# Optimization experiments

Hardware: AMD Instinct MI355X
Metric: run time of the kernel (lower is better)

The kernel has to match this reference:

```python
import jax, jax.numpy as jnp
import numpy as np

N_NODES = 100000


def gcn_layer(x, src, dst, W, b):
    """PyG GCNConv: add self-loops, symmetric deg normalization, XW then scatter-add."""
    n = x.shape[0]
    loop = jnp.arange(n, dtype=src.dtype)
    s = jnp.concatenate([src, loop])
    d = jnp.concatenate([dst, loop])
    # degree of target nodes (includes self-loop)
    deg = jax.ops.segment_sum(jnp.ones_like(d, dtype=x.dtype), d, num_segments=n)
    dinv = jnp.where(deg > 0, jax.lax.rsqrt(deg), 0.0)
    norm = dinv[s] * dinv[d]                      # [E+N]
    h = x @ W                                     # [N, out]
    msg = h[s] * norm[:, None]                    # [E+N, out]
    out = jax.ops.segment_sum(msg, d, num_segments=n) + b
    return out


def setup_inputs() -> dict:
    key = jax.random.key(0)
    k1, k2, k3, k4 = jax.random.split(key, 4)
    d_in, d_hid, d_out = 256, 256, 128
    E = 3200000
    x = jax.random.normal(k1, (N_NODES, d_in), dtype=jnp.float32)
    edge_index = jax.random.randint(k2, (2, E), 0, N_NODES, dtype=jnp.int64)
    # glorot-style init for GCN weights
    W1 = jax.random.normal(k3, (d_in, d_hid), dtype=jnp.float32) / np.sqrt(d_in)
    b1 = jnp.zeros((d_hid,), dtype=jnp.float32)
    W2 = jax.random.normal(k4, (d_hid, d_out), dtype=jnp.float32) / np.sqrt(d_hid)
    b2 = jnp.zeros((d_out,), dtype=jnp.float32)
    return {"x": x, "W1": W1, "b1": b1, "W2": W2, "b2": b2, "edge_index": edge_index}


def reference(x, W1, b1, W2, b2, edge_index):
    src, dst = edge_index[0], edge_index[1]
    h = jax.nn.relu(gcn_layer(x, src, dst, W1, b1))
    out = jax.nn.relu(gcn_layer(h, src, dst, W2, b2))
    return out
```

## Files before the change

kernel.cpp:

```cpp
#include <hip/hip_runtime.h>


typedef short          s16x8 __attribute__((ext_vector_type(8)));
typedef float          f32x4 __attribute__((ext_vector_type(4)));
typedef unsigned short u16x8 __attribute__((ext_vector_type(8)));
typedef unsigned short u16x4 __attribute__((ext_vector_type(4)));

__device__ __forceinline__ float bf2f(unsigned short u) {
  union { unsigned int i; float f; } x; x.i = ((unsigned int)u) << 16; return x.f;
}
__device__ __forceinline__ unsigned short f2bf(float f) {
  union { float f; unsigned int i; } x; x.f = f;
  unsigned int r = x.i + 0x7FFFu + ((x.i >> 16) & 1u);
  return (unsigned short)(r >> 16);
}


#define NBUCK_PAD 1024
#define BIN_CHUNK 8192

__global__ __launch_bounds__(256) void k_hist(const int* __restrict__ dst,
                                              int* __restrict__ bcnt, int E) {
  __shared__ int h[NBUCK_PAD];
  int t = threadIdx.x;
  for (int i = t; i < NBUCK_PAD; i += 256) h[i] = 0;
  __syncthreads();
  int stride = gridDim.x * 256;
  for (int e = blockIdx.x * 256 + t; e < E; e += stride) atomicAdd(&h[dst[e] >> 7], 1);
  __syncthreads();
  for (int i = t; i < NBUCK_PAD; i += 256) {
    int v = h[i];
    if (v) atomicAdd(bcnt + i, v);
  }
}

__global__ void k_bscan(const int* __restrict__ bcnt, int* __restrict__ bptr,
                        int* __restrict__ bcur, int* __restrict__ rowptr, int M, int E) {
  __shared__ int sh[NBUCK_PAD];
  int t = threadIdx.x;
  int v = bcnt[t];
  sh[t] = v; __syncthreads();
  int x = v;
  for (int off = 1; off < NBUCK_PAD; off <<= 1) {
    int y = (t >= off) ? sh[t - off] : 0;
    __syncthreads();
    x += y; sh[t] = x;
    __syncthreads();
  }
  bptr[t] = x - v;
  bcur[t] = x - v;
  if (t == NBUCK_PAD - 1) bptr[NBUCK_PAD] = x;
  if (t == 0) rowptr[M] = E;
}

__global__ __launch_bounds__(256) void k_bin(const int* __restrict__ src,
                                             const int* __restrict__ dst,
                                             int* __restrict__ bcur,
                                             unsigned int* __restrict__ binned, int E) {
  __shared__ int hist[NBUCK_PAD];
  __shared__ int base[NBUCK_PAD];
  int t = threadIdx.x;
  int e0 = blockIdx.x * BIN_CHUNK;
  int e1 = min(e0 + BIN_CHUNK, E);
  for (int i = t; i < NBUCK_PAD; i += 256) hist[i] = 0;
  __syncthreads();
  for (int e = e0 + t; e < e1; e += 256) atomicAdd(&hist[dst[e] >> 7], 1);
  __syncthreads();
  for (int i = t; i < NBUCK_PAD; i += 256) {
    int h = hist[i];
    base[i] = h ? atomicAdd(bcur + i, h) : 0;
    hist[i] = 0;
  }
  __syncthreads();
  for (int e = e0 + t; e < e1; e += 256) {
    int d = dst[e], s = src[e];
    int b = d >> 7;
    int p = base[b] + atomicAdd(&hist[b], 1);
    binned[p] = ((unsigned)(d & 127) << 17) | (unsigned)s;
  }
}

__global__ __launch_bounds__(256) void k_csr(const unsigned int* __restrict__ binned,
                                             const int* __restrict__ bptr,
                                             int* __restrict__ rowptr,
                                             float* __restrict__ dinv,
                                             int* __restrict__ col, int M) {
  __shared__ int deg[128];
  __shared__ int sc[128];
  __shared__ int cur[128];
  int b = blockIdx.x, t = threadIdx.x;
  int n0 = b << 7;
  int nn = min(128, M - n0);
  int e0 = bptr[b], e1 = bptr[b + 1];
  if (t < 128) deg[t] = 0;
  __syncthreads();
  for (int e = e0 + t; e < e1; e += 256) atomicAdd(&deg[(binned[e] >> 17) & 127], 1);
  __syncthreads();
  if (t < 128) sc[t] = deg[t];
  __syncthreads();
  for (int off = 1; off < 128; off <<= 1) {
    int y = 0;
    if (t < 128 && t >= off) y = sc[t - off];
    __syncthreads();
    if (t < 128) sc[t] += y;
    __syncthreads();
  }
  if (t < nn) {
    int excl = sc[t] - deg[t];
    rowptr[n0 + t] = e0 + excl;
    dinv[n0 + t] = rsqrtf((float)(deg[t] + 1));
    cur[t] = excl;
  }
  __syncthreads();
  for (int e = e0 + t; e < e1; e += 256) {
    unsigned v = binned[e];
    int dl = (v >> 17) & 127;
    int p = e0 + atomicAdd(&cur[dl], 1);
    col[p] = (int)(v & 0x1FFFFu);
  }
}


__global__ void k_cvt_w(const float* __restrict__ W1, const float* __restrict__ W2,
                        unsigned short* __restrict__ w1t, unsigned short* __restrict__ w2t) {
  int i = blockIdx.x * 256 + threadIdx.x;
  if (i < 256 * 256) {
    int k = i >> 8, n = i & 255;
    w1t[n * 256 + k] = f2bf(W1[i]);
  } else {
    int j = i - 256 * 256;
    if (j < 256 * 128) {
      int k = j >> 7, n = j & 127;
      w2t[n * 256 + k] = f2bf(W2[j]);
    }
  }
}


__device__ __forceinline__ int swz4(int row, int kc) { return kc ^ ((row & 3) << 3); }

__global__ __launch_bounds__(512) void k_gemm1(
    const float* __restrict__ X, const unsigned short* __restrict__ Bt,
    const float* __restrict__ dinv, unsigned short* __restrict__ G, int M) {
  const int K = 256;
  __shared__ short lA[128 * 32];
  __shared__ short lB[256 * 32];
  int tid = threadIdx.x;
  int wid = tid >> 6, lane = tid & 63;
  int wm = wid >> 2, wn = wid & 3;
  int l15 = lane & 15;
  int lkg = (lane >> 4) * 8;
  int bm = blockIdx.x * 128;

  f32x4 acc[4][4] = {};

  for (int kt = 0; kt < 8; ++kt) {
    int k0 = kt * 32;
    __syncthreads();
#pragma unroll
    for (int h = 0; h < 2; ++h) {
      int cid = tid + h * 512;
      int r = cid >> 3, c4 = (cid & 7) * 4;
      int gr = bm + r;
      float4 v = {0.f, 0.f, 0.f, 0.f};
      if (gr < M) v = *(const float4*)(X + (size_t)gr * K + k0 + c4);
      u16x4 o; o[0] = f2bf(v.x); o[1] = f2bf(v.y); o[2] = f2bf(v.z); o[3] = f2bf(v.w);
      *(u16x4*)(&lA[r * 32 + swz4(r, c4)]) = o;
    }
#pragma unroll
    for (int h = 0; h < 2; ++h) {
      int cid = tid + h * 512;
      int n = cid >> 2, kc = (cid & 3) * 8;
      s16x8 v = *(const s16x8*)(Bt + (size_t)n * K + k0 + kc);
      *(s16x8*)(&lB[n * 32 + swz4(n, kc)]) = v;
    }
    __syncthreads();

    s16x8 af[4], bfr[4];
#pragma unroll
    for (int mi = 0; mi < 4; ++mi) {
      int r = wm * 64 + mi * 16 + l15;
      af[mi] = *(const s16x8*)(&lA[r * 32 + swz4(r, lkg)]);
    }
#pragma unroll
    for (int ni = 0; ni < 4; ++ni) {
      int c = wn * 64 + ni * 16 + l15;
      bfr[ni] = *(const s16x8*)(&lB[c * 32 + swz4(c, lkg)]);
    }
#pragma unroll
    for (int mi = 0; mi < 4; ++mi)
#pragma unroll
      for (int ni = 0; ni < 4; ++ni)
        acc[mi][ni] = __builtin_amdgcn_mfma_f32_16x16x32_bf16(af[mi], bfr[ni], acc[mi][ni], 0, 0, 0);
  }

#pragma unroll
  for (int mi = 0; mi < 4; ++mi) {
    int mrow0 = bm + wm * 64 + mi * 16 + (lane >> 4) * 4;
#pragma unroll
    for (int j = 0; j < 4; ++j) {
      int m = mrow0 + j;
      if (m < M) {
        float dv = dinv[m];
#pragma unroll
        for (int ni = 0; ni < 4; ++ni)
          G[(size_t)m * 256 + wn * 64 + ni * 16 + l15] = f2bf(acc[mi][ni][j] * dv);
      }
    }
  }
}


__global__ __launch_bounds__(512) void k_gemm2(
    const unsigned short* __restrict__ A, const unsigned short* __restrict__ Bt,
    const float* __restrict__ dinv, unsigned short* __restrict__ G, int M) {
  const int K = 256;
  __shared__ short lA[128 * 32];
  __shared__ short lB[128 * 32];
  int tid = threadIdx.x;
  int wid = tid >> 6, lane = tid & 63;
  int wm = wid >> 2, wn = wid & 3;
  int l15 = lane & 15;
  int lkg = (lane >> 4) * 8;
  int bm = blockIdx.x * 128;

  f32x4 acc[4][2] = {};

  for (int kt = 0; kt < 8; ++kt) {
    int k0 = kt * 32;
    __syncthreads();
    {
      int r = tid >> 2, kc = (tid & 3) * 8;
      int gr = bm + r;
      s16x8 v = {0, 0, 0, 0, 0, 0, 0, 0};
      if (gr < M) v = *(const s16x8*)(A + (size_t)gr * K + k0 + kc);
      *(s16x8*)(&lA[r * 32 + swz4(r, kc)]) = v;
    }
    {
      int n = tid >> 2, kc = (tid & 3) * 8;
      s16x8 v = *(const s16x8*)(Bt + (size_t)n * K + k0 + kc);
      *(s16x8*)(&lB[n * 32 + swz4(n, kc)]) = v;
    }
    __syncthreads();

    s16x8 af[4], bfr[2];
#pragma unroll
    for (int mi = 0; mi < 4; ++mi) {
      int r = wm * 64 + mi * 16 + l15;
      af[mi] = *(const s16x8*)(&lA[r * 32 + swz4(r, lkg)]);
    }
#pragma unroll
    for (int ni = 0; ni < 2; ++ni) {
      int c = wn * 32 + ni * 16 + l15;
      bfr[ni] = *(const s16x8*)(&lB[c * 32 + swz4(c, lkg)]);
    }
#pragma unroll
    for (int mi = 0; mi < 4; ++mi)
#pragma unroll
      for (int ni = 0; ni < 2; ++ni)
        acc[mi][ni] = __builtin_amdgcn_mfma_f32_16x16x32_bf16(af[mi], bfr[ni], acc[mi][ni], 0, 0, 0);
  }

#pragma unroll
  for (int mi = 0; mi < 4; ++mi) {
    int mrow0 = bm + wm * 64 + mi * 16 + (lane >> 4) * 4;
#pragma unroll
    for (int j = 0; j < 4; ++j) {
      int m = mrow0 + j;
      if (m < M) {
        float dv = dinv[m];
#pragma unroll
        for (int ni = 0; ni < 2; ++ni)
          G[(size_t)m * 128 + wn * 32 + ni * 16 + l15] = f2bf(acc[mi][ni][j] * dv);
      }
    }
  }
}


__global__ __launch_bounds__(256) void k_agg256(
    const unsigned short* __restrict__ G, const int* __restrict__ rowptr,
    const int* __restrict__ col, const float* __restrict__ dinv,
    const float* __restrict__ bias, unsigned short* __restrict__ H, int M) {
  int lane = threadIdx.x & 63;
  int v = (blockIdx.x << 2) + (threadIdx.x >> 6);
  if (v >= M) return;
  int half = lane >> 5;
  int l32 = lane & 31;
  int c8 = l32 * 8;
  float a[8] = {};
  if (half == 0) {
    u16x8 s = *(const u16x8*)(G + (size_t)v * 256 + c8);
#pragma unroll
    for (int i = 0; i < 8; ++i) a[i] += bf2f(s[i]);
  }
  int jb = rowptr[v], je = rowptr[v + 1];
  int j = jb;
  for (; j + 7 < je; j += 8) {
    int u0 = col[j + half];
    int u1 = col[j + 2 + half];
    int u2 = col[j + 4 + half];
    int u3 = col[j + 6 + half];
    u16x8 p0 = *(const u16x8*)(G + (size_t)u0 * 256 + c8);
    u16x8 p1 = *(const u16x8*)(G + (size_t)u1 * 256 + c8);
    u16x8 p2 = *(const u16x8*)(G + (size_t)u2 * 256 + c8);
    u16x8 p3 = *(const u16x8*)(G + (size_t)u3 * 256 + c8);
#pragma unroll
    for (int i = 0; i < 8; ++i)
      a[i] += (bf2f(p0[i]) + bf2f(p1[i])) + (bf2f(p2[i]) + bf2f(p3[i]));
  }
  for (; j + 1 < je; j += 2) {
    int u = col[j + half];
    u16x8 p = *(const u16x8*)(G + (size_t)u * 256 + c8);
#pragma unroll
    for (int i = 0; i < 8; ++i) a[i] += bf2f(p[i]);
  }
  if (j < je && half == 0) {
    int u = col[j];
    u16x8 p = *(const u16x8*)(G + (size_t)u * 256 + c8);
#pragma unroll
    for (int i = 0; i < 8; ++i) a[i] += bf2f(p[i]);
  }
#pragma unroll
  for (int i = 0; i < 8; ++i) a[i] += __shfl_xor(a[i], 32, 64);
  if (half == 0) {
    float dv = dinv[v];
    float4 b0 = *(const float4*)(bias + c8);
    float4 b1 = *(const float4*)(bias + c8 + 4);
    u16x8 o;
    o[0] = f2bf(fmaxf(fmaf(dv, a[0], b0.x), 0.f));
    o[1] = f2bf(fmaxf(fmaf(dv, a[1], b0.y), 0.f));
    o[2] = f2bf(fmaxf(fmaf(dv, a[2], b0.z), 0.f));
    o[3] = f2bf(fmaxf(fmaf(dv, a[3], b0.w), 0.f));
    o[4] = f2bf(fmaxf(fmaf(dv, a[4], b1.x), 0.f));
    o[5] = f2bf(fmaxf(fmaf(dv, a[5], b1.y), 0.f));
    o[6] = f2bf(fmaxf(fmaf(dv, a[6], b1.z), 0.f));
    o[7] = f2bf(fmaxf(fmaf(dv, a[7], b1.w), 0.f));
    *(u16x8*)(H + (size_t)v * 256 + c8) = o;
  }
}

__global__ __launch_bounds__(256) void k_agg128(
    const unsigned short* __restrict__ G, const int* __restrict__ rowptr,
    const int* __restrict__ col, const float* __restrict__ dinv,
    const float* __restrict__ bias, float* __restrict__ Out, int M) {
  int lane = threadIdx.x & 63;
  int v = (blockIdx.x << 2) + (threadIdx.x >> 6);
  if (v >= M) return;
  int half = lane >> 5;
  int l32 = lane & 31;
  int c4 = l32 * 4;
  float a[4] = {};
  if (half == 0) {
    u16x4 s = *(const u16x4*)(G + (size_t)v * 128 + c4);
#pragma unroll
    for (int i = 0; i < 4; ++i) a[i] += bf2f(s[i]);
  }
  int jb = rowptr[v], je = rowptr[v + 1];
  int j = jb;
  for (; j + 7 < je; j += 8) {
    int u0 = col[j + half];
    int u1 = col[j + 2 + half];
    int u2 = col[j + 4 + half];
    int u3 = col[j + 6 + half];
    u16x4 p0 = *(const u16x4*)(G + (size_t)u0 * 128 + c4);
    u16x4 p1 = *(const u16x4*)(G + (size_t)u1 * 128 + c4);
    u16x4 p2 = *(const u16x4*)(G + (size_t)u2 * 128 + c4);
    u16x4 p3 = *(const u16x4*)(G + (size_t)u3 * 128 + c4);
#pragma unroll
    for (int i = 0; i < 4; ++i)
      a[i] += (bf2f(p0[i]) + bf2f(p1[i])) + (bf2f(p2[i]) + bf2f(p3[i]));
  }
  for (; j + 1 < je; j += 2) {
    int u = col[j + half];
    u16x4 p = *(const u16x4*)(G + (size_t)u * 128 + c4);
#pragma unroll
    for (int i = 0; i < 4; ++i) a[i] += bf2f(p[i]);
  }
  if (j < je && half == 0) {
    int u = col[j];
    u16x4 p = *(const u16x4*)(G + (size_t)u * 128 + c4);
#pragma unroll
    for (int i = 0; i < 4; ++i) a[i] += bf2f(p[i]);
  }
#pragma unroll
  for (int i = 0; i < 4; ++i) a[i] += __shfl_xor(a[i], 32, 64);
  if (half == 0) {
    float dv = dinv[v];
    float4 bb = *(const float4*)(bias + c4);
    float4 r;
    r.x = fmaxf(fmaf(dv, a[0], bb.x), 0.f);
    r.y = fmaxf(fmaf(dv, a[1], bb.y), 0.f);
    r.z = fmaxf(fmaf(dv, a[2], bb.z), 0.f);
    r.w = fmaxf(fmaf(dv, a[3], bb.w), 0.f);
    *(float4*)(Out + (size_t)v * 128 + c4) = r;
  }
}


extern "C" void kernel_launch(void* const* d_in, const int* in_sizes, int n_in,
                              void* d_out, int out_size, void* d_ws, size_t ws_size,
                              hipStream_t stream) {
  const float* x  = (const float*)d_in[0];
  const float* W1 = (const float*)d_in[1];
  const float* b1 = (const float*)d_in[2];
  const float* W2 = (const float*)d_in[3];
  const float* b2 = (const float*)d_in[4];
  const int*   ei = (const int*)d_in[5];

  const int D_IN = 256, D_HID = 256, D_OUT = 128;
  const int M = in_sizes[0] / D_IN;
  const int E = in_sizes[5] / 2;
  const int* src = ei;
  const int* dst = ei + E;

  char* p = (char*)d_ws;
  auto alloc = [&](size_t bytes) { void* r = (void*)p; p += (bytes + 255) & ~(size_t)255; return r; };
  float* dinv = (float*)alloc((size_t)M * 4);
  int* rowptr = (int*)alloc((size_t)(M + 1) * 4);
  int* bcnt   = (int*)alloc(NBUCK_PAD * 4);
  int* bptr   = (int*)alloc((NBUCK_PAD + 1) * 4);
  int* bcur   = (int*)alloc(NBUCK_PAD * 4);
  int* colx   = (int*)alloc((size_t)E * 4);
  unsigned short* w1t = (unsigned short*)alloc((size_t)D_HID * D_IN * 2);
  unsigned short* w2t = (unsigned short*)alloc((size_t)D_OUT * D_HID * 2);
  unsigned short* g1  = (unsigned short*)alloc((size_t)M * D_HID * 2);
  unsigned short* hid = (unsigned short*)alloc((size_t)M * D_HID * 2);
  unsigned short* g2  = (unsigned short*)alloc((size_t)M * D_OUT * 2);
  unsigned int* binned = (unsigned int*)g1;

  int nbuck = (M + 127) >> 7;
  int nbin  = (E + BIN_CHUNK - 1) / BIN_CHUNK;

  hipMemsetAsync(bcnt, 0, NBUCK_PAD * 4, stream);
  k_hist <<<256, 256, 0, stream>>>(dst, bcnt, E);
  k_bscan<<<1, NBUCK_PAD, 0, stream>>>(bcnt, bptr, bcur, rowptr, M, E);
  k_bin  <<<nbin, 256, 0, stream>>>(src, dst, bcur, binned, E);
  k_csr  <<<nbuck, 256, 0, stream>>>(binned, bptr, rowptr, dinv, colx, M);

  k_cvt_w<<<(256 * 256 + 256 * 128 + 255) / 256, 256, 0, stream>>>(W1, W2, w1t, w2t);

  k_gemm1 <<<nbuck, 512, 0, stream>>>(x, w1t, dinv, g1, M);
  k_agg256<<<(M + 3) / 4, 256, 0, stream>>>(g1, rowptr, colx, dinv, b1, hid, M);
  k_gemm2 <<<nbuck, 512, 0, stream>>>(hid, w2t, dinv, g2, M);
  k_agg128<<<(M + 3) / 4, 256, 0, stream>>>(g2, rowptr, colx, dinv, b2, (float*)d_out, M);
}
```

Baseline: 537.8 us.

## Store GEMM outputs in 16-feature slices and aggregate per slice for cache locality

The GEMMs now write G in a sliced layout, [slice][node][16], so each 16-feature slice of all nodes is contiguous (3.2 MB per slice for 100k nodes). New aggregation kernels are scheduled so that concurrent blocks work on a few slices over neighbouring node chunks, which keeps each slice's working set cache-resident during the random neighbour gathers. The cost is that every gather is only 32 bytes per edge, col indices are re-read once per slice (16x or 8x more index traffic), and each wave needs three shuffle reductions per node.

```diff
diff --git a/kernel.cpp b/kernel.cpp
--- a/kernel.cpp
+++ b/kernel.cpp
@@ -3,8 +3,8 @@
 
 typedef short          s16x8 __attribute__((ext_vector_type(8)));
 typedef float          f32x4 __attribute__((ext_vector_type(4)));
-typedef unsigned short u16x8 __attribute__((ext_vector_type(8)));
 typedef unsigned short u16x4 __attribute__((ext_vector_type(4)));
+typedef unsigned short u16x2 __attribute__((ext_vector_type(2)));
 
 __device__ __forceinline__ float bf2f(unsigned short u) {
   union { unsigned int i; float f; } x; x.i = ((unsigned int)u) << 16; return x.f;
@@ -203,9 +203,71 @@
       if (m < M) {
         float dv = dinv[m];
 #pragma unroll
-        for (int ni = 0; ni < 4; ++ni)
-          G[(size_t)m * 256 + wn * 64 + ni * 16 + l15] = f2bf(acc[mi][ni][j] * dv);
+        for (int ni = 0; ni < 4; ++ni) {
+          int slice = wn * 4 + ni;
+          G[(size_t)slice * M * 16 + (size_t)m * 16 + l15] = f2bf(acc[mi][ni][j] * dv);
+        }
       }
+    }
+  }
+}
+
+
+__global__ __launch_bounds__(256) void k_agg256s(
+    const unsigned short* __restrict__ G, const int* __restrict__ rowptr,
+    const int* __restrict__ col, const float* __restrict__ dinv,
+    const float* __restrict__ bias, unsigned short* __restrict__ H,
+    int M, int nb) {
+  int b = blockIdx.x;
+  int phase = b / (8 * nb);
+  int rem = b - phase * (8 * nb);
+  int chunk = rem >> 3;
+  int slice = phase * 8 + (b & 7);
+  int tid = threadIdx.x;
+  int w = tid >> 6, lane = tid & 63;
+  int fl = lane & 7;
+  int eg = lane >> 3;
+  const unsigned short* Gs = G + (size_t)slice * M * 16;
+  int fo = fl * 2;
+  float bb0 = bias[slice * 16 + fo];
+  float bb1 = bias[slice * 16 + fo + 1];
+  int v0 = chunk * 64 + w * 16;
+
+  for (int n = 0; n < 16; ++n) {
+    int v = v0 + n;
+    if (v >= M) break;
+    float a0 = 0.f, a1 = 0.f;
+    if (eg == 0) {
+      u16x2 s = *(const u16x2*)(Gs + (size_t)v * 16 + fo);
+      a0 = bf2f(s[0]); a1 = bf2f(s[1]);
+    }
+    int jb = rowptr[v], je = rowptr[v + 1];
+    int base = jb;
+    for (; base + 16 <= je; base += 16) {
+      int u1 = col[base + eg];
+      int u2 = col[base + 8 + eg];
+      u16x2 p1 = *(const u16x2*)(Gs + (size_t)u1 * 16 + fo);
+      u16x2 p2 = *(const u16x2*)(Gs + (size_t)u2 * 16 + fo);
+      a0 += bf2f(p1[0]) + bf2f(p2[0]);
+      a1 += bf2f(p1[1]) + bf2f(p2[1]);
+    }
+    for (; base < je; base += 8) {
+      int idx = base + eg;
+      if (idx < je) {
+        int u = col[idx];
+        u16x2 p = *(const u16x2*)(Gs + (size_t)u * 16 + fo);
+        a0 += bf2f(p[0]); a1 += bf2f(p[1]);
+      }
+    }
+    a0 += __shfl_xor(a0, 8, 64);  a1 += __shfl_xor(a1, 8, 64);
+    a0 += __shfl_xor(a0, 16, 64); a1 += __shfl_xor(a1, 16, 64);
+    a0 += __shfl_xor(a0, 32, 64); a1 += __shfl_xor(a1, 32, 64);
+    if (eg == 0) {
+      float dv = dinv[v];
+      u16x2 o;
+      o[0] = f2bf(fmaxf(fmaf(dv, a0, bb0), 0.f));
+      o[1] = f2bf(fmaxf(fmaf(dv, a1, bb1), 0.f));
+      *(u16x2*)(H + (size_t)v * 256 + slice * 16 + fo) = o;
     }
   }
 }
@@ -270,130 +332,69 @@
       if (m < M) {
         float dv = dinv[m];
 #pragma unroll
-        for (int ni = 0; ni < 2; ++ni)
-          G[(size_t)m * 128 + wn * 32 + ni * 16 + l15] = f2bf(acc[mi][ni][j] * dv);
+        for (int ni = 0; ni < 2; ++ni) {
+          int slice = wn * 2 + ni;
+          G[(size_t)slice * M * 16 + (size_t)m * 16 + l15] = f2bf(acc[mi][ni][j] * dv);
+        }
       }
     }
   }
 }
 
 
-__global__ __launch_bounds__(256) void k_agg256(
-    const unsigned short* __restrict__ G, const int* __restrict__ rowptr,
-    const int* __restrict__ col, const float* __restrict__ dinv,
-    const float* __restrict__ bias, unsigned short* __restrict__ H, int M) {
-  int lane = threadIdx.x & 63;
-  int v = (blockIdx.x << 2) + (threadIdx.x >> 6);
-  if (v >= M) return;
-  int half = lane >> 5;
-  int l32 = lane & 31;
-  int c8 = l32 * 8;
-  float a[8] = {};
-  if (half == 0) {
-    u16x8 s = *(const u16x8*)(G + (size_t)v * 256 + c8);
-#pragma unroll
-    for (int i = 0; i < 8; ++i) a[i] += bf2f(s[i]);
-  }
-  int jb = rowptr[v], je = rowptr[v + 1];
-  int j = jb;
-  for (; j + 7 < je; j += 8) {
-    int u0 = col[j + half];
-    int u1 = col[j + 2 + half];
-    int u2 = col[j + 4 + half];
-    int u3 = col[j + 6 + half];
-    u16x8 p0 = *(const u16x8*)(G + (size_t)u0 * 256 + c8);
-    u16x8 p1 = *(const u16x8*)(G + (size_t)u1 * 256 + c8);
-    u16x8 p2 = *(const u16x8*)(G + (size_t)u2 * 256 + c8);
-    u16x8 p3 = *(const u16x8*)(G + (size_t)u3 * 256 + c8);
-#pragma unroll
-    for (int i = 0; i < 8; ++i)
-      a[i] += (bf2f(p0[i]) + bf2f(p1[i])) + (bf2f(p2[i]) + bf2f(p3[i]));
-  }
-  for (; j + 1 < je; j += 2) {
-    int u = col[j + half];
-    u16x8 p = *(const u16x8*)(G + (size_t)u * 256 + c8);
-#pragma unroll
-    for (int i = 0; i < 8; ++i) a[i] += bf2f(p[i]);
-  }
-  if (j < je && half == 0) {
-    int u = col[j];
-    u16x8 p = *(const u16x8*)(G + (size_t)u * 256 + c8);
-#pragma unroll
-    for (int i = 0; i < 8; ++i) a[i] += bf2f(p[i]);
-  }
-#pragma unroll
-  for (int i = 0; i < 8; ++i) a[i] += __shfl_xor(a[i], 32, 64);
-  if (half == 0) {
-    float dv = dinv[v];
-    float4 b0 = *(const float4*)(bias + c8);
-    float4 b1 = *(const float4*)(bias + c8 + 4);
-    u16x8 o;
-    o[0] = f2bf(fmaxf(fmaf(dv, a[0], b0.x), 0.f));
-    o[1] = f2bf(fmaxf(fmaf(dv, a[1], b0.y), 0.f));
-    o[2] = f2bf(fmaxf(fmaf(dv, a[2], b0.z), 0.f));
-    o[3] = f2bf(fmaxf(fmaf(dv, a[3], b0.w), 0.f));
-    o[4] = f2bf(fmaxf(fmaf(dv, a[4], b1.x), 0.f));
-    o[5] = f2bf(fmaxf(fmaf(dv, a[5], b1.y), 0.f));
-    o[6] = f2bf(fmaxf(fmaf(dv, a[6], b1.z), 0.f));
-    o[7] = f2bf(fmaxf(fmaf(dv, a[7], b1.w), 0.f));
-    *(u16x8*)(H + (size_t)v * 256 + c8) = o;
-  }
-}
-
-__global__ __launch_bounds__(256) void k_agg128(
+__global__ __launch_bounds__(256) void k_agg128s(
     const unsigned short* __restrict__ G, const int* __restrict__ rowptr,
     const int* __restrict__ col, const float* __restrict__ dinv,
     const float* __restrict__ bias, float* __restrict__ Out, int M) {
-  int lane = threadIdx.x & 63;
-  int v = (blockIdx.x << 2) + (threadIdx.x >> 6);
-  if (v >= M) return;
-  int half = lane >> 5;
-  int l32 = lane & 31;
-  int c4 = l32 * 4;
-  float a[4] = {};
-  if (half == 0) {
-    u16x4 s = *(const u16x4*)(G + (size_t)v * 128 + c4);
-#pragma unroll
-    for (int i = 0; i < 4; ++i) a[i] += bf2f(s[i]);
-  }
-  int jb = rowptr[v], je = rowptr[v + 1];
-  int j = jb;
-  for (; j + 7 < je; j += 8) {
-    int u0 = col[j + half];
-    int u1 = col[j + 2 + half];
-    int u2 = col[j + 4 + half];
-    int u3 = col[j + 6 + half];
-    u16x4 p0 = *(const u16x4*)(G + (size_t)u0 * 128 + c4);
-    u16x4 p1 = *(const u16x4*)(G + (size_t)u1 * 128 + c4);
-    u16x4 p2 = *(const u16x4*)(G + (size_t)u2 * 128 + c4);
-    u16x4 p3 = *(const u16x4*)(G + (size_t)u3 * 128 + c4);
-#pragma unroll
-    for (int i = 0; i < 4; ++i)
-      a[i] += (bf2f(p0[i]) + bf2f(p1[i])) + (bf2f(p2[i]) + bf2f(p3[i]));
-  }
-  for (; j + 1 < je; j += 2) {
-    int u = col[j + half];
-    u16x4 p = *(const u16x4*)(G + (size_t)u * 128 + c4);
-#pragma unroll
-    for (int i = 0; i < 4; ++i) a[i] += bf2f(p[i]);
-  }
-  if (j < je && half == 0) {
-    int u = col[j];
-    u16x4 p = *(const u16x4*)(G + (size_t)u * 128 + c4);
-#pragma unroll
-    for (int i = 0; i < 4; ++i) a[i] += bf2f(p[i]);
-  }
-#pragma unroll
-  for (int i = 0; i < 4; ++i) a[i] += __shfl_xor(a[i], 32, 64);
-  if (half == 0) {
-    float dv = dinv[v];
-    float4 bb = *(const float4*)(bias + c4);
-    float4 r;
-    r.x = fmaxf(fmaf(dv, a[0], bb.x), 0.f);
-    r.y = fmaxf(fmaf(dv, a[1], bb.y), 0.f);
-    r.z = fmaxf(fmaf(dv, a[2], bb.z), 0.f);
-    r.w = fmaxf(fmaf(dv, a[3], bb.w), 0.f);
-    *(float4*)(Out + (size_t)v * 128 + c4) = r;
+  int b = blockIdx.x;
+  int chunk = b >> 3;
+  int slice = b & 7;
+  int tid = threadIdx.x;
+  int w = tid >> 6, lane = tid & 63;
+  int fl = lane & 7;
+  int eg = lane >> 3;
+  const unsigned short* Gs = G + (size_t)slice * M * 16;
+  int fo = fl * 2;
+  float bb0 = bias[slice * 16 + fo];
+  float bb1 = bias[slice * 16 + fo + 1];
+  int v0 = chunk * 64 + w * 16;
+
+  for (int n = 0; n < 16; ++n) {
+    int v = v0 + n;
+    if (v >= M) break;
+    float a0 = 0.f, a1 = 0.f;
+    if (eg == 0) {
+      u16x2 s = *(const u16x2*)(Gs + (size_t)v * 16 + fo);
+      a0 = bf2f(s[0]); a1 = bf2f(s[1]);
+    }
+    int jb = rowptr[v], je = rowptr[v + 1];
+    int base = jb;
+    for (; base + 16 <= je; base += 16) {
+      int u1 = col[base + eg];
+      int u2 = col[base + 8 + eg];
+      u16x2 p1 = *(const u16x2*)(Gs + (size_t)u1 * 16 + fo);
+      u16x2 p2 = *(const u16x2*)(Gs + (size_t)u2 * 16 + fo);
+      a0 += bf2f(p1[0]) + bf2f(p2[0]);
+      a1 += bf2f(p1[1]) + bf2f(p2[1]);
+    }
+    for (; base < je; base += 8) {
+      int idx = base + eg;
+      if (idx < je) {
+        int u = col[idx];
+        u16x2 p = *(const u16x2*)(Gs + (size_t)u * 16 + fo);
+        a0 += bf2f(p[0]); a1 += bf2f(p[1]);
+      }
+    }
+    a0 += __shfl_xor(a0, 8, 64);  a1 += __shfl_xor(a1, 8, 64);
+    a0 += __shfl_xor(a0, 16, 64); a1 += __shfl_xor(a1, 16, 64);
+    a0 += __shfl_xor(a0, 32, 64); a1 += __shfl_xor(a1, 32, 64);
+    if (eg == 0) {
+      float dv = dinv[v];
+      float2 r;
+      r.x = fmaxf(fmaf(dv, a0, bb0), 0.f);
+      r.y = fmaxf(fmaf(dv, a1, bb1), 0.f);
+      *(float2*)(Out + (size_t)v * 128 + slice * 16 + fo) = r;
+    }
   }
 }
 
@@ -431,6 +432,7 @@
 
   int nbuck = (M + 127) >> 7;
   int nbin  = (E + BIN_CHUNK - 1) / BIN_CHUNK;
+  int nb    = (M + 63) / 64;
 
   hipMemsetAsync(bcnt, 0, NBUCK_PAD * 4, stream);
   k_hist <<<256, 256, 0, stream>>>(dst, bcnt, E);
@@ -440,8 +442,8 @@
 
   k_cvt_w<<<(256 * 256 + 256 * 128 + 255) / 256, 256, 0, stream>>>(W1, W2, w1t, w2t);
 
-  k_gemm1 <<<nbuck, 512, 0, stream>>>(x, w1t, dinv, g1, M);
-  k_agg256<<<(M + 3) / 4, 256, 0, stream>>>(g1, rowptr, colx, dinv, b1, hid, M);
-  k_gemm2 <<<nbuck, 512, 0, stream>>>(hid, w2t, dinv, g2, M);
-  k_agg128<<<(M + 3) / 4, 256, 0, stream>>>(g2, rowptr, colx, dinv, b2, (float*)d_out, M);
-}
+  k_gemm1  <<<nbuck, 512, 0, stream>>>(x, w1t, dinv, g1, M);
+  k_agg256s<<<2 * 8 * nb, 256, 0, stream>>>(g1, rowptr, colx, dinv, b1, hid, M, nb);
+  k_gemm2  <<<nbuck, 512, 0, stream>>>(hid, w2t, dinv, g2, M);
+  k_agg128s<<<8 * nb, 256, 0, stream>>>(g2, rowptr, colx, dinv, b2, (float*)d_out, M);
+}
```

Measured after the change: 1.081 ms. 101% more time.

## Split gathered feature matrices into column halves and aggregate each half separately

Applied to the files above, without the earlier changes.

The GEMM epilogues now write G in two column-half planes, and aggregation runs as two passes, one per half. The intent is to halve the working set of each gather pass (12.8MB/6.4MB instead of 25.6MB/12.8MB) so the randomly gathered rows stay in L2/MALL cache, and to use more edge slots per wavefront. The histogram kernel also switches to int4 vectorized loads, and BIN_CHUNK is halved. The cost is extra kernel launches, a second pass over the CSR indices, and more shuffle reductions.

```diff
diff --git a/kernel.cpp b/kernel.cpp
--- a/kernel.cpp
+++ b/kernel.cpp
@@ -17,7 +17,7 @@
 
 
 #define NBUCK_PAD 1024
-#define BIN_CHUNK 8192
+#define BIN_CHUNK 4096
 
 __global__ __launch_bounds__(256) void k_hist(const int* __restrict__ dst,
                                               int* __restrict__ bcnt, int E) {
@@ -25,8 +25,19 @@
   int t = threadIdx.x;
   for (int i = t; i < NBUCK_PAD; i += 256) h[i] = 0;
   __syncthreads();
+  int n4 = E >> 2;
   int stride = gridDim.x * 256;
-  for (int e = blockIdx.x * 256 + t; e < E; e += stride) atomicAdd(&h[dst[e] >> 7], 1);
+  const int4* d4 = (const int4*)dst;
+  for (int e = blockIdx.x * 256 + t; e < n4; e += stride) {
+    int4 v = d4[e];
+    atomicAdd(&h[v.x >> 7], 1);
+    atomicAdd(&h[v.y >> 7], 1);
+    atomicAdd(&h[v.z >> 7], 1);
+    atomicAdd(&h[v.w >> 7], 1);
+  }
+  if (blockIdx.x == 0) {
+    for (int e = n4 * 4 + t; e < E; e += 256) atomicAdd(&h[dst[e] >> 7], 1);
+  }
   __syncthreads();
   for (int i = t; i < NBUCK_PAD; i += 256) {
     int v = h[i];
@@ -204,7 +215,8 @@
         float dv = dinv[m];
 #pragma unroll
         for (int ni = 0; ni < 4; ++ni)
-          G[(size_t)m * 256 + wn * 64 + ni * 16 + l15] = f2bf(acc[mi][ni][j] * dv);
+          G[(size_t)(wn >> 1) * M * 128 + (size_t)m * 128 + (wn & 1) * 64 + ni * 16 + l15]
+              = f2bf(acc[mi][ni][j] * dv);
       }
     }
   }
@@ -271,129 +283,129 @@
         float dv = dinv[m];
 #pragma unroll
         for (int ni = 0; ni < 2; ++ni)
-          G[(size_t)m * 128 + wn * 32 + ni * 16 + l15] = f2bf(acc[mi][ni][j] * dv);
+          G[(size_t)(wn >> 1) * M * 64 + (size_t)m * 64 + (wn & 1) * 32 + ni * 16 + l15]
+              = f2bf(acc[mi][ni][j] * dv);
       }
     }
   }
 }
 
 
-__global__ __launch_bounds__(256) void k_agg256(
+__global__ __launch_bounds__(256) void k_agg256h(
     const unsigned short* __restrict__ G, const int* __restrict__ rowptr,
     const int* __restrict__ col, const float* __restrict__ dinv,
-    const float* __restrict__ bias, unsigned short* __restrict__ H, int M) {
+    const float* __restrict__ bias, unsigned short* __restrict__ H,
+    int M, int phase) {
   int lane = threadIdx.x & 63;
   int v = (blockIdx.x << 2) + (threadIdx.x >> 6);
   if (v >= M) return;
-  int half = lane >> 5;
-  int l32 = lane & 31;
-  int c8 = l32 * 8;
+  int slot = lane >> 4;
+  int f8 = (lane & 15) * 8;
   float a[8] = {};
-  if (half == 0) {
-    u16x8 s = *(const u16x8*)(G + (size_t)v * 256 + c8);
+  if (slot == 0) {
+    u16x8 s = *(const u16x8*)(G + (size_t)v * 128 + f8);
 #pragma unroll
     for (int i = 0; i < 8; ++i) a[i] += bf2f(s[i]);
   }
   int jb = rowptr[v], je = rowptr[v + 1];
   int j = jb;
-  for (; j + 7 < je; j += 8) {
-    int u0 = col[j + half];
-    int u1 = col[j + 2 + half];
-    int u2 = col[j + 4 + half];
-    int u3 = col[j + 6 + half];
-    u16x8 p0 = *(const u16x8*)(G + (size_t)u0 * 256 + c8);
-    u16x8 p1 = *(const u16x8*)(G + (size_t)u1 * 256 + c8);
-    u16x8 p2 = *(const u16x8*)(G + (size_t)u2 * 256 + c8);
-    u16x8 p3 = *(const u16x8*)(G + (size_t)u3 * 256 + c8);
-#pragma unroll
-    for (int i = 0; i < 8; ++i)
-      a[i] += (bf2f(p0[i]) + bf2f(p1[i])) + (bf2f(p2[i]) + bf2f(p3[i]));
-  }
-  for (; j + 1 < je; j += 2) {
-    int u = col[j + half];
-    u16x8 p = *(const u16x8*)(G + (size_t)u * 256 + c8);
+  for (; j + 8 <= je; j += 8) {
+    int u0 = col[j + slot];
+    int u1 = col[j + 4 + slot];
+    u16x8 p0 = *(const u16x8*)(G + (size_t)u0 * 128 + f8);
+    u16x8 p1 = *(const u16x8*)(G + (size_t)u1 * 128 + f8);
+#pragma unroll
+    for (int i = 0; i < 8; ++i) a[i] += bf2f(p0[i]) + bf2f(p1[i]);
+  }
+  for (; j + 4 <= je; j += 4) {
+    int u = col[j + slot];
+    u16x8 p = *(const u16x8*)(G + (size_t)u * 128 + f8);
 #pragma unroll
     for (int i = 0; i < 8; ++i) a[i] += bf2f(p[i]);
   }
-  if (j < je && half == 0) {
-    int u = col[j];
-    u16x8 p = *(const u16x8*)(G + (size_t)u * 256 + c8);
+  int rem = je - j;
+  if (slot < rem) {
+    int u = col[j + slot];
+    u16x8 p = *(const u16x8*)(G + (size_t)u * 128 + f8);
 #pragma unroll
     for (int i = 0; i < 8; ++i) a[i] += bf2f(p[i]);
   }
 #pragma unroll
-  for (int i = 0; i < 8; ++i) a[i] += __shfl_xor(a[i], 32, 64);
-  if (half == 0) {
+  for (int i = 0; i < 8; ++i) {
+    a[i] += __shfl_xor(a[i], 16, 64);
+    a[i] += __shfl_xor(a[i], 32, 64);
+  }
+  if (lane < 16) {
     float dv = dinv[v];
-    float4 b0 = *(const float4*)(bias + c8);
-    float4 b1 = *(const float4*)(bias + c8 + 4);
+    const float* bp = bias + phase * 128 + f8;
     u16x8 o;
-    o[0] = f2bf(fmaxf(fmaf(dv, a[0], b0.x), 0.f));
-    o[1] = f2bf(fmaxf(fmaf(dv, a[1], b0.y), 0.f));
-    o[2] = f2bf(fmaxf(fmaf(dv, a[2], b0.z), 0.f));
-    o[3] = f2bf(fmaxf(fmaf(dv, a[3], b0.w), 0.f));
-    o[4] = f2bf(fmaxf(fmaf(dv, a[4], b1.x), 0.f));
-    o[5] = f2bf(fmaxf(fmaf(dv, a[5], b1.y), 0.f));
-    o[6] = f2bf(fmaxf(fmaf(dv, a[6], b1.z), 0.f));
-    o[7] = f2bf(fmaxf(fmaf(dv, a[7], b1.w), 0.f));
-    *(u16x8*)(H + (size_t)v * 256 + c8) = o;
-  }
-}
-
-__global__ __launch_bounds__(256) void k_agg128(
+#pragma unroll
+    for (int i = 0; i < 8; ++i) o[i] = f2bf(fmaxf(fmaf(dv, a[i], bp[i]), 0.f));
+    *(u16x8*)(H + (size_t)v * 256 + phase * 128 + f8) = o;
+  }
+}
+
+
+__global__ __launch_bounds__(256) void k_agg128h(
     const unsigned short* __restrict__ G, const int* __restrict__ rowptr,
     const int* __restrict__ col, const float* __restrict__ dinv,
-    const float* __restrict__ bias, float* __restrict__ Out, int M) {
+    const float* __restrict__ bias, float* __restrict__ Out,
+    int M, int phase) {
   int lane = threadIdx.x & 63;
   int v = (blockIdx.x << 2) + (threadIdx.x >> 6);
   if (v >= M) return;
-  int half = lane >> 5;
-  int l32 = lane & 31;
-  int c4 = l32 * 4;
-  float a[4] = {};
-  if (half == 0) {
-    u16x4 s = *(const u16x4*)(G + (size_t)v * 128 + c4);
-#pragma unroll
-    for (int i = 0; i < 4; ++i) a[i] += bf2f(s[i]);
+  int slot = lane >> 3;
+  int f8 = (lane & 7) * 8;
+  float a[8] = {};
+  if (slot == 0) {
+    u16x8 s = *(const u16x8*)(G + (size_t)v * 64 + f8);
+#pragma unroll
+    for (int i = 0; i < 8; ++i) a[i] += bf2f(s[i]);
   }
   int jb = rowptr[v], je = rowptr[v + 1];
   int j = jb;
-  for (; j + 7 < je; j += 8) {
-    int u0 = col[j + half];
-    int u1 = col[j + 2 + half];
-    int u2 = col[j + 4 + half];
-    int u3 = col[j + 6 + half];
-    u16x4 p0 = *(const u16x4*)(G + (size_t)u0 * 128 + c4);
-    u16x4 p1 = *(const u16x4*)(G + (size_t)u1 * 128 + c4);
-    u16x4 p2 = *(const u16x4*)(G + (size_t)u2 * 128 + c4);
-    u16x4 p3 = *(const u16x4*)(G + (size_t)u3 * 128 + c4);
-#pragma unroll
-    for (int i = 0; i < 4; ++i)
-      a[i] += (bf2f(p0[i]) + bf2f(p1[i])) + (bf2f(p2[i]) + bf2f(p3[i]));
-  }
-  for (; j + 1 < je; j += 2) {
-    int u = col[j + half];
-    u16x4 p = *(const u16x4*)(G + (size_t)u * 128 + c4);
-#pragma unroll
-    for (int i = 0; i < 4; ++i) a[i] += bf2f(p[i]);
-  }
-  if (j < je && half == 0) {
-    int u = col[j];
-    u16x4 p = *(const u16x4*)(G + (size_t)u * 128 + c4);
-#pragma unroll
-    for (int i = 0; i < 4; ++i) a[i] += bf2f(p[i]);
-  }
-#pragma unroll
-  for (int i = 0; i < 4; ++i) a[i] += __shfl_xor(a[i], 32, 64);
-  if (half == 0) {
+  for (; j + 16 <= je; j += 16) {
+    int u0 = col[j + slot];
+    int u1 = col[j + 8 + slot];
+    u16x8 p0 = *(const u16x8*)(G + (size_t)u0 * 64 + f8);
+    u16x8 p1 = *(const u16x8*)(G + (size_t)u1 * 64 + f8);
+#pragma unroll
+    for (int i = 0; i < 8; ++i) a[i] += bf2f(p0[i]) + bf2f(p1[i]);
+  }
+  for (; j + 8 <= je; j += 8) {
+    int u = col[j + slot];
+    u16x8 p = *(const u16x8*)(G + (size_t)u * 64 + f8);
+#pragma unroll
+    for (int i = 0; i < 8; ++i) a[i] += bf2f(p[i]);
+  }
+  int rem = je - j;
+  if (slot < rem) {
+    int u = col[j + slot];
+    u16x8 p = *(const u16x8*)(G + (size_t)u * 64 + f8);
+#pragma unroll
+    for (int i = 0; i < 8; ++i) a[i] += bf2f(p[i]);
+  }
+#pragma unroll
+  for (int i = 0; i < 8; ++i) {
+    a[i] += __shfl_xor(a[i], 8, 64);
+    a[i] += __shfl_xor(a[i], 16, 64);
+    a[i] += __shfl_xor(a[i], 32, 64);
+  }
+  if (lane < 8) {
     float dv = dinv[v];
-    float4 bb = *(const float4*)(bias + c4);
-    float4 r;
-    r.x = fmaxf(fmaf(dv, a[0], bb.x), 0.f);
-    r.y = fmaxf(fmaf(dv, a[1], bb.y), 0.f);
-    r.z = fmaxf(fmaf(dv, a[2], bb.z), 0.f);
-    r.w = fmaxf(fmaf(dv, a[3], bb.w), 0.f);
-    *(float4*)(Out + (size_t)v * 128 + c4) = r;
+    const float* bp = bias + phase * 64 + f8;
+    float4 r0, r1;
+    r0.x = fmaxf(fmaf(dv, a[0], bp[0]), 0.f);
+    r0.y = fmaxf(fmaf(dv, a[1], bp[1]), 0.f);
+    r0.z = fmaxf(fmaf(dv, a[2], bp[2]), 0.f);
+    r0.w = fmaxf(fmaf(dv, a[3], bp[3]), 0.f);
+    r1.x = fmaxf(fmaf(dv, a[4], bp[4]), 0.f);
+    r1.y = fmaxf(fmaf(dv, a[5], bp[5]), 0.f);
+    r1.z = fmaxf(fmaf(dv, a[6], bp[6]), 0.f);
+    r1.w = fmaxf(fmaf(dv, a[7], bp[7]), 0.f);
+    float* op = Out + (size_t)v * 128 + phase * 64 + f8;
+    *(float4*)op = r0;
+    *(float4*)(op + 4) = r1;
   }
 }
 
@@ -431,6 +443,7 @@
 
   int nbuck = (M + 127) >> 7;
   int nbin  = (E + BIN_CHUNK - 1) / BIN_CHUNK;
+  int nb4   = (M + 3) / 4;
 
   hipMemsetAsync(bcnt, 0, NBUCK_PAD * 4, stream);
   k_hist <<<256, 256, 0, stream>>>(dst, bcnt, E);
@@ -440,8 +453,10 @@
 
   k_cvt_w<<<(256 * 256 + 256 * 128 + 255) / 256, 256, 0, stream>>>(W1, W2, w1t, w2t);
 
-  k_gemm1 <<<nbuck, 512, 0, stream>>>(x, w1t, dinv, g1, M);
-  k_agg256<<<(M + 3) / 4, 256, 0, stream>>>(g1, rowptr, colx, dinv, b1, hid, M);
-  k_gemm2 <<<nbuck, 512, 0, stream>>>(hid, w2t, dinv, g2, M);
-  k_agg128<<<(M + 3) / 4, 256, 0, stream>>>(g2, rowptr, colx, dinv, b2, (float*)d_out, M);
-}
+  k_gemm1  <<<nbuck, 512, 0, stream>>>(x, w1t, dinv, g1, M);
+  k_agg256h<<<nb4, 256, 0, stream>>>(g1,                      rowptr, colx, dinv, b1, hid, M, 0);
+  k_agg256h<<<nb4, 256, 0, stream>>>(g1 + (size_t)M * 128,    rowptr, colx, dinv, b1, hid, M, 1);
+  k_gemm2  <<<nbuck, 512, 0, stream>>>(hid, w2t, dinv, g2, M);
+  k_agg128h<<<nb4, 256, 0, stream>>>(g2,                      rowptr, colx, dinv, b2, (float*)d_out, M, 0);
+  k_agg128h<<<nb4, 256, 0, stream>>>(g2 + (size_t)M * 64,     rowptr, colx, dinv, b2, (float*)d_out, M, 1);
+}
```

Result: no change. 540.3 us (+0.5%).
